# Kernel optimization log

Measured on AMD Instinct MI355X. Metric: run time of the kernel, lower is better.

## Reference

```python
import jax, jax.numpy as jnp
import numpy as np

B, T, C, H, K = 16, 8192, 128, 128, 5


def setup_inputs() -> dict:
    key = jax.random.key(0)
    ks = jax.random.split(key, 6)
    std = 1.0 / np.sqrt(H)  # matches reset_parameters uniform(-std, std)
    u = lambda k, s: jax.random.uniform(k, s, jnp.float32, -std, std)
    return {
        "inputs": jax.random.normal(ks[0], (B, T, C), jnp.float32),
        "init_state": jax.random.normal(ks[1], (2, B, H), jnp.float32),
        "z_w": u(ks[2], (H, C, K)),
        "z_b": u(ks[3], (H,)),
        "f_w": u(ks[4], (H, C, K)),
        "f_b": u(ks[5], (H,)),
    }


def _conv1d_same(x, w, b):
    # x: (B, C, T), w: (H, C, K) -> (B, H, T), padding='same'
    y = jax.lax.conv_general_dilated(
        x, w, window_strides=(1,), padding="SAME",
        dimension_numbers=("NCH", "OIH", "NCH"))
    return y + b[None, :, None]


def reference(inputs, init_state, z_w, z_b, f_w, f_b):
    # inputs: (B, T, C); init_state: (2, B, H)
    x = jnp.transpose(inputs, (0, 2, 1))                       # (B, C, T)
    raw_f = jnp.transpose(_conv1d_same(x, f_w, f_b), (0, 2, 1))  # (B, T, H)
    raw_z = jnp.transpose(_conv1d_same(x, z_w, z_b), (0, 2, 1))  # (B, T, H)
    # prepend init state along time -> (B, T+1, H)
    raw_f = jnp.concatenate([init_state[0][:, None, :], raw_f], axis=1)
    raw_z = jnp.concatenate([init_state[1][:, None, :], raw_z], axis=1)
    log_one_minus_f = jax.nn.log_sigmoid(-raw_f)  # mode='f'
    log_z = jax.nn.log_sigmoid(raw_z)
    log_f = jax.nn.log_sigmoid(raw_f)
    cs = jnp.cumsum(log_f, axis=1)
    # recurrent_gates[t] = log_f[t] - cumsum[t] + cumsum[-1]
    rg = log_f - cs + cs[:, -1:, :]
    log_hidden = jax.lax.cumlogsumexp(log_z + log_one_minus_f + rg, axis=1)
    return jnp.exp(log_hidden - rg)  # (B, T+1, H)
```

## Files before the change

### kernel.cpp

```cpp
#include <hip/hip_runtime.h>
#include <hip/hip_bf16.h>
#include <cstdint>

#define DEVFN __device__ __forceinline__

namespace {

constexpr int B = 16, T = 8192, C = 128, H = 128, K = 5;
constexpr int TP1 = T + 1;
constexpr int N = B * TP1 * H;
constexpr int NKK = 20;
constexpr int NCH = T / 64;
constexpr int NSER = B * H;
constexpr int WF_ELE = NKK * 8 * 64 * 2 * 8;
constexpr int XPITCH = 136;

typedef __attribute__((ext_vector_type(8))) short short8;
typedef __attribute__((ext_vector_type(4))) float f32x4;

DEVFN float sigmoidf(float x) { return 1.0f / (1.0f + __expf(-x)); }
DEVFN unsigned bfb(float v) {
  __hip_bfloat16 h = __float2bfloat16(v);
  return (unsigned)*reinterpret_cast<unsigned short*>(&h);
}

DEVFN void compose(float& P, float& Q, float& Fl, float Pr, float Qr, float Flr) {
  float t = Fl * Pr;
  P = P * t;
  Q = fmaf(t, Q, Qr);
  Fl = Flr;
}

__global__ __launch_bounds__(256)
void wprep_kernel(const float* __restrict__ fw, const float* __restrict__ zw,
                  short* __restrict__ Wfrag) {
  int idx = blockIdx.x * 256 + threadIdx.x;
  if (idx >= WF_ELE) return;
  int j = idx & 7;
  int fz = (idx >> 3) & 1;
  int lane = (idx >> 4) & 63;
  int nf8 = (idx >> 10) & 7;
  int kk = idx >> 13;
  int kdim = kk * 32 + ((lane >> 4) << 3) + j;
  int h = nf8 * 16 + (lane & 15);
  int k = kdim >> 7, c = kdim & 127;
  int src = (h * C + c) * K + k;
  float w = fz ? zw[src] : fw[src];
  Wfrag[idx] = (short)bfb(w);
}

__global__ __launch_bounds__(512, 4)
void conv_mfma_kernel(const float* __restrict__ x,
                      const float* __restrict__ fb, const float* __restrict__ zb,
                      const short* __restrict__ Wfrag,
                      unsigned* __restrict__ FG,
                      float* __restrict__ sumP, float* __restrict__ sumQ) {
  __shared__ short xs[68 * XPITCH];
  const int b = blockIdx.y;
  const int t0 = blockIdx.x * 64;
  const int tid = threadIdx.x;
  const int lane = tid & 63;
  const int wid = tid >> 6;
  const int lrow = lane & 15;
  const int lg = lane >> 4;

  for (int i = tid; i < 68 * 16; i += 512) {
    int r = i >> 4, co = (i & 15) << 3;
    int t = t0 - 2 + r;
    f32x4 v0 = {0.f, 0.f, 0.f, 0.f}, v1 = v0;
    if (t >= 0 && t < T) {
      const f32x4* p = reinterpret_cast<const f32x4*>(x + ((size_t)(b * T + t)) * C + co);
      v0 = p[0]; v1 = p[1];
    }
    short8 s;
    s[0] = (short)bfb(v0[0]); s[1] = (short)bfb(v0[1]); s[2] = (short)bfb(v0[2]); s[3] = (short)bfb(v0[3]);
    s[4] = (short)bfb(v1[0]); s[5] = (short)bfb(v1[1]); s[6] = (short)bfb(v1[2]); s[7] = (short)bfb(v1[3]);
    *reinterpret_cast<short8*>(xs + r * XPITCH + co) = s;
  }
  __syncthreads();

  f32x4 accF[4], accZ[4];
#pragma unroll
  for (int mf = 0; mf < 4; ++mf) { accF[mf] = {0.f,0.f,0.f,0.f}; accZ[mf] = {0.f,0.f,0.f,0.f}; }

  const char* xsb = reinterpret_cast<const char*>(xs);
  const short8* wb = reinterpret_cast<const short8*>(Wfrag) + (wid * 128 + lane * 2);
  const int abase = lrow * 272 + lg * 16;

  short8 wf[4], wz[4], av[2][4];
#pragma unroll
  for (int p = 0; p < 3; ++p) {
    wf[p] = wb[p * 1024];
    wz[p] = wb[p * 1024 + 1];
  }
#pragma unroll
  for (int mf = 0; mf < 4; ++mf)
    av[0][mf] = *reinterpret_cast<const short8*>(xsb + (abase + (mf * 16) * 272));

#pragma unroll
  for (int kk = 0; kk < NKK; ++kk) {
    __builtin_amdgcn_sched_barrier(0);
    if (kk + 3 < NKK) {
      const int o = (kk + 3) * 1024;
      wf[(kk + 3) & 3] = wb[o];
      wz[(kk + 3) & 3] = wb[o + 1];
    }
    if (kk + 1 < NKK) {
      const int k1 = (kk + 1) >> 2;
      const int cq1 = ((kk + 1) & 3) << 6;
#pragma unroll
      for (int mf = 0; mf < 4; ++mf)
        av[(kk + 1) & 1][mf] =
            *reinterpret_cast<const short8*>(xsb + (abase + (mf * 16 + k1) * 272 + cq1));
    }
    __builtin_amdgcn_sched_barrier(0);
#pragma unroll
    for (int mf = 0; mf < 4; ++mf) {
      accF[mf] = __builtin_amdgcn_mfma_f32_16x16x32_bf16(av[kk & 1][mf], wf[kk & 3], accF[mf], 0, 0, 0);
      accZ[mf] = __builtin_amdgcn_mfma_f32_16x16x32_bf16(av[kk & 1][mf], wz[kk & 3], accZ[mf], 0, 0, 0);
    }
  }

  const int cblk = blockIdx.x;
  const int h = wid * 16 + lrow;
  const float biasF = fb[h], biasZ = zb[h];
  float cP = 1.f, cQ = 0.f, cFl = 1.f;
#pragma unroll
  for (int mf = 0; mf < 4; ++mf) {
    float y = 0.f, P = 1.f, prevF = 1.f;
#pragma unroll
    for (int j = 0; j < 4; ++j) {
      int m = mf * 16 + lg * 4 + j;
      int s = t0 + m + 1;
      float rf = accF[mf][j] + biasF;
      float rz = accZ[mf][j] + biasZ;
      float F = sigmoidf(rf);
      float G = sigmoidf(rz) * (1.0f - F);
      FG[(size_t)(b * TP1 + s) * H + h] = bfb(F) | (bfb(G) << 16);
      if (j == 0) { y = G; P = 1.f; }
      else { P *= prevF; y = fmaf(prevF, y, G); }
      prevF = F;
    }
    float tP = P, tQ = y, tFl = prevF;
    {
      float pP = __shfl(tP, lane + 16, 64);
      float pQ = __shfl(tQ, lane + 16, 64);
      float pF = __shfl(tFl, lane + 16, 64);
      compose(tP, tQ, tFl, pP, pQ, pF);
      pP = __shfl(tP, lane + 32, 64);
      pQ = __shfl(tQ, lane + 32, 64);
      pF = __shfl(tFl, lane + 32, 64);
      compose(tP, tQ, tFl, pP, pQ, pF);
    }
    if (mf == 0) { cP = tP; cQ = tQ; cFl = tFl; }
    else compose(cP, cQ, cFl, tP, tQ, tFl);
  }
  if (lg == 0) {
    int sidx = cblk * NSER + b * H + h;
    sumP[sidx] = cP;
    sumQ[sidx] = cQ;
  }
}

__global__ void scanB_kernel(const float* __restrict__ init,
                             const unsigned* __restrict__ FG_r,
                             unsigned* __restrict__ FG_w,
                             const float* __restrict__ sumQ,
                             float* __restrict__ sumP_cin,
                             float* __restrict__ out) {
  int g = blockIdx.x * blockDim.x + threadIdx.x;
  int b = g >> 7, h = g & (H - 1);
  float rf = init[g];
  float rz = init[NSER + g];
  float F0 = sigmoidf(rf), z = sigmoidf(rz);
  float G0 = z * (1.0f - F0);
  size_t base = (size_t)b * TP1 * H + h;
  FG_w[base] = bfb(F0) | (bfb(G0) << 16);
  out[base] = G0;
  float y = G0;
  float prevFl = F0;
  for (int j = 0; j < NCH; ++j) {
    int sidx = j * NSER + g;
    float Ps = sumP_cin[sidx];
    float Q  = sumQ[sidx];
    sumP_cin[sidx] = y;
    y = fmaf(prevFl * Ps, y, Q);
    if (j + 1 < NCH)
      prevFl = __uint_as_float(FG_r[base + (size_t)(64 * (j + 1)) * H] << 16);
  }
}

__global__ __launch_bounds__(128)
void scanC_kernel(const unsigned* __restrict__ FG, const float* __restrict__ cin,
                  float* __restrict__ out) {
  const int b = blockIdx.y, j = blockIdx.x, h = threadIdx.x;
  const int s0 = 1 + j * 64;
  float y = cin[j * NSER + b * H + h];
  const size_t base = (size_t)b * TP1 * H + h;
  const unsigned* p = FG + base + (size_t)s0 * H;
  float Fprev = __uint_as_float(p[-H] << 16);
  float* po = out + base + (size_t)s0 * H;
#pragma unroll 8
  for (int t = 0; t < 64; ++t) {
    unsigned u = *p; p += H;
    float G = __uint_as_float(u & 0xffff0000u);
    y = fmaf(Fprev, y, G);
    Fprev = __uint_as_float(u << 16);
    *po = y; po += H;
  }
}

}

extern "C" void kernel_launch(void* const* d_in, const int* in_sizes, int n_in,
                              void* d_out, int out_size, void* d_ws, size_t ws_size,
                              hipStream_t stream) {
  const float* x    = (const float*)d_in[0];
  const float* init = (const float*)d_in[1];
  const float* zw   = (const float*)d_in[2];
  const float* zb   = (const float*)d_in[3];
  const float* fw   = (const float*)d_in[4];
  const float* fb   = (const float*)d_in[5];
  float* out = (float*)d_out;
  char* ws = (char*)d_ws;

  unsigned* FG = (unsigned*)ws;
  float* sumP = (float*)(ws + (size_t)N * 4);
  float* sumQ = sumP + (size_t)NCH * NSER;
  short* Wfrag = (short*)(sumQ + (size_t)NCH * NSER);

  wprep_kernel<<<(WF_ELE + 255) / 256, 256, 0, stream>>>(fw, zw, Wfrag);
  conv_mfma_kernel<<<dim3(NCH, B), 512, 0, stream>>>(x, fb, zb, Wfrag, FG, sumP, sumQ);
  scanB_kernel<<<16, 128, 0, stream>>>(init, FG, FG, sumQ, sumP, out);
  scanC_kernel<<<dim3(NCH, B), 128, 0, stream>>>(FG, sumP, out);
}
```

Measured before the change: 100.3 us.

## Fuse conv, chunk scan and apply into one cooperative kernel with grid syncs

Replaces the three-kernel conv/scanB/scanC sequence with a single cooperative kernel of 512 blocks. Each block computes four 64-step chunks, prefetching the next chunk's input into a double-buffered LDS tile. Grid syncs separate the conv phase, a serial carry scan over chunks done by four blocks, and the per-chunk apply phase. This removes kernel launch gaps and the extra FG reread in scanB. The cost is two grid-wide barriers, a serial scan running on only four blocks while the rest of the grid waits, and a dependence on cooperative-launch occupancy, with the old three-kernel path kept as a fallback.

Result: no change. 100.1 us (-0.2%).

```diff
diff --git a/kernel.cpp b/kernel.cpp
--- a/kernel.cpp
+++ b/kernel.cpp
@@ -1,5 +1,6 @@
 #include <hip/hip_runtime.h>
 #include <hip/hip_bf16.h>
+#include <hip/hip_cooperative_groups.h>
 #include <cstdint>
 
 #define DEVFN __device__ __forceinline__
@@ -14,6 +15,7 @@
 constexpr int NSER = B * H;
 constexpr int WF_ELE = NKK * 8 * 64 * 2 * 8;
 constexpr int XPITCH = 136;
+constexpr int XHALF = 68 * XPITCH;
 
 typedef __attribute__((ext_vector_type(8))) short short8;
 typedef __attribute__((ext_vector_type(4))) float f32x4;
@@ -47,6 +49,195 @@
   int src = (h * C + c) * K + k;
   float w = fz ? zw[src] : fw[src];
   Wfrag[idx] = (short)bfb(w);
+}
+
+DEVFN void stage_issue(const float* __restrict__ xp, int b, int t0, int tid,
+                       f32x4& a0, f32x4& b0, f32x4& a1, f32x4& b1,
+                       f32x4& a2, f32x4& b2) {
+  auto ld = [&](int i, f32x4& va, f32x4& vb) {
+    int r = i >> 4, co = (i & 15) << 3;
+    int t = t0 - 2 + r;
+    va = {0.f, 0.f, 0.f, 0.f}; vb = va;
+    if (t >= 0 && t < T) {
+      const f32x4* p = reinterpret_cast<const f32x4*>(xp + ((size_t)(b * T + t)) * C + co);
+      va = p[0]; vb = p[1];
+    }
+  };
+  ld(tid, a0, b0);
+  ld(tid + 512, a1, b1);
+  if (tid < 64) ld(tid + 1024, a2, b2);
+}
+DEVFN void stage_write(short* xsbuf, int tid,
+                       f32x4& a0, f32x4& b0, f32x4& a1, f32x4& b1,
+                       f32x4& a2, f32x4& b2) {
+  auto st = [&](int i, f32x4& va, f32x4& vb) {
+    int r = i >> 4, co = (i & 15) << 3;
+    short8 s;
+    s[0] = (short)bfb(va[0]); s[1] = (short)bfb(va[1]); s[2] = (short)bfb(va[2]); s[3] = (short)bfb(va[3]);
+    s[4] = (short)bfb(vb[0]); s[5] = (short)bfb(vb[1]); s[6] = (short)bfb(vb[2]); s[7] = (short)bfb(vb[3]);
+    *reinterpret_cast<short8*>(xsbuf + r * XPITCH + co) = s;
+  };
+  st(tid, a0, b0);
+  st(tid + 512, a1, b1);
+  if (tid < 64) st(tid + 1024, a2, b2);
+}
+
+__global__ __launch_bounds__(512, 4)
+void fused_kernel(const float* __restrict__ x,
+                  const float* __restrict__ fb, const float* __restrict__ zb,
+                  const float* __restrict__ initst,
+                  const short* __restrict__ Wfrag,
+                  float2* __restrict__ stat,
+                  unsigned* __restrict__ FG,
+                  float* __restrict__ out) {
+  __shared__ short xs[2 * XHALF];
+  const int bid = blockIdx.x;
+  const int b = bid >> 5;
+  const int q = bid & 31;
+  const int tid = threadIdx.x;
+  const int lane = tid & 63;
+  const int wid = tid >> 6;
+  const int lrow = lane & 15;
+  const int lg = lane >> 4;
+
+  const short8* wb = reinterpret_cast<const short8*>(Wfrag) + (wid * 128 + lane * 2);
+  const int abase = lrow * 272 + lg * 16;
+  const int h = wid * 16 + lrow;
+  const float biasF = fb[h], biasZ = zb[h];
+
+  f32x4 p0a, p0b, p1a, p1b, p2a, p2b;
+
+  stage_issue(x, b, q * 256, tid, p0a, p0b, p1a, p1b, p2a, p2b);
+  stage_write(xs, tid, p0a, p0b, p1a, p1b, p2a, p2b);
+  __syncthreads();
+
+#pragma unroll 1
+  for (int c = 0; c < 4; ++c) {
+    const int t0 = (q * 4 + c) * 64;
+    const char* xsb = reinterpret_cast<const char*>(xs + (c & 1) * XHALF);
+
+    f32x4 accF[4], accZ[4];
+#pragma unroll
+    for (int mf = 0; mf < 4; ++mf) { accF[mf] = {0.f,0.f,0.f,0.f}; accZ[mf] = {0.f,0.f,0.f,0.f}; }
+
+    short8 wf[4], wz[4], av[2][4];
+#pragma unroll
+    for (int p = 0; p < 3; ++p) {
+      wf[p] = wb[p * 1024];
+      wz[p] = wb[p * 1024 + 1];
+    }
+#pragma unroll
+    for (int mf = 0; mf < 4; ++mf)
+      av[0][mf] = *reinterpret_cast<const short8*>(xsb + (abase + (mf * 16) * 272));
+
+#pragma unroll
+    for (int kk = 0; kk < NKK; ++kk) {
+      __builtin_amdgcn_sched_barrier(0);
+      if (kk + 3 < NKK) {
+        const int o = (kk + 3) * 1024;
+        wf[(kk + 3) & 3] = wb[o];
+        wz[(kk + 3) & 3] = wb[o + 1];
+      }
+      if (kk + 1 < NKK) {
+        const int k1 = (kk + 1) >> 2;
+        const int cq1 = ((kk + 1) & 3) << 6;
+#pragma unroll
+        for (int mf = 0; mf < 4; ++mf)
+          av[(kk + 1) & 1][mf] =
+              *reinterpret_cast<const short8*>(xsb + (abase + (mf * 16 + k1) * 272 + cq1));
+      }
+      __builtin_amdgcn_sched_barrier(0);
+#pragma unroll
+      for (int mf = 0; mf < 4; ++mf) {
+        accF[mf] = __builtin_amdgcn_mfma_f32_16x16x32_bf16(av[kk & 1][mf], wf[kk & 3], accF[mf], 0, 0, 0);
+        accZ[mf] = __builtin_amdgcn_mfma_f32_16x16x32_bf16(av[kk & 1][mf], wz[kk & 3], accZ[mf], 0, 0, 0);
+      }
+    }
+
+    if (c < 3)
+      stage_issue(x, b, t0 + 64, tid, p0a, p0b, p1a, p1b, p2a, p2b);
+    __builtin_amdgcn_sched_barrier(0);
+
+    float cP = 1.f, cQ = 0.f, cFl = 1.f;
+#pragma unroll
+    for (int mf = 0; mf < 4; ++mf) {
+      float y = 0.f, P = 1.f, prevF = 1.f;
+#pragma unroll
+      for (int j = 0; j < 4; ++j) {
+        int m = mf * 16 + lg * 4 + j;
+        int s = t0 + m + 1;
+        float F = sigmoidf(accF[mf][j] + biasF);
+        float G = sigmoidf(accZ[mf][j] + biasZ) * (1.0f - F);
+        FG[(size_t)(b * TP1 + s) * H + h] = bfb(F) | (bfb(G) << 16);
+        if (j == 0) { y = G; P = 1.f; }
+        else { P *= prevF; y = fmaf(prevF, y, G); }
+        prevF = F;
+      }
+      float tP = P, tQ = y, tFl = prevF;
+      {
+        float pP = __shfl(tP, lane + 16, 64);
+        float pQ = __shfl(tQ, lane + 16, 64);
+        float pF = __shfl(tFl, lane + 16, 64);
+        compose(tP, tQ, tFl, pP, pQ, pF);
+        pP = __shfl(tP, lane + 32, 64);
+        pQ = __shfl(tQ, lane + 32, 64);
+        pF = __shfl(tFl, lane + 32, 64);
+        compose(tP, tQ, tFl, pP, pQ, pF);
+      }
+      if (mf == 0) { cP = tP; cQ = tQ; cFl = tFl; }
+      else compose(cP, cQ, cFl, tP, tQ, tFl);
+    }
+    if (lg == 0)
+      stat[(size_t)(b * NCH + q * 4 + c) * H + h] = make_float2(cP, cQ);
+
+    if (c < 3) {
+      __syncthreads();
+      stage_write(xs + ((c + 1) & 1) * XHALF, tid, p0a, p0b, p1a, p1b, p2a, p2b);
+      __syncthreads();
+    }
+  }
+
+  cooperative_groups::this_grid().sync();
+
+  if (bid < 4) {
+    int g = bid * 512 + tid;
+    int b2 = g >> 7, h2 = g & (H - 1);
+    float F0 = sigmoidf(initst[g]);
+    float z0 = sigmoidf(initst[NSER + g]);
+    float G0 = z0 * (1.0f - F0);
+    size_t base = (size_t)b2 * TP1 * H + h2;
+    out[base] = G0;
+    float y = G0, Fp = F0;
+    for (int j = 0; j < NCH; ++j) {
+      size_t sidx = (size_t)(b2 * NCH + j) * H + h2;
+      float2 pq = stat[sidx];
+      stat[sidx] = make_float2(y, Fp);
+      y = fmaf(Fp * pq.x, y, pq.y);
+      if (j + 1 < NCH)
+        Fp = __uint_as_float(FG[base + (size_t)(64 * (j + 1)) * H] << 16);
+    }
+  }
+
+  cooperative_groups::this_grid().sync();
+
+  {
+    const int sub = tid >> 7;
+    const int h3 = tid & (H - 1);
+    const int j = q * 4 + sub;
+    float2 cf = stat[(size_t)(b * NCH + j) * H + h3];
+    float y = cf.x, Fprev = cf.y;
+    size_t base = (size_t)b * TP1 * H + h3;
+    const unsigned* p = FG + base + (size_t)(1 + j * 64) * H;
+    float* po = out + base + (size_t)(1 + j * 64) * H;
+#pragma unroll 8
+    for (int t = 0; t < 64; ++t) {
+      unsigned u = *p; p += H;
+      float G = __uint_as_float(u & 0xffff0000u);
+      y = fmaf(Fprev, y, G);
+      Fprev = __uint_as_float(u << 16);
+      *po = y; po += H;
+    }
+  }
 }
 
 __global__ __launch_bounds__(512, 4)
@@ -224,13 +415,26 @@
   float* out = (float*)d_out;
   char* ws = (char*)d_ws;
 
-  unsigned* FG = (unsigned*)ws;
-  float* sumP = (float*)(ws + (size_t)N * 4);
-  float* sumQ = sumP + (size_t)NCH * NSER;
-  short* Wfrag = (short*)(sumQ + (size_t)NCH * NSER);
+  unsigned* FG  = (unsigned*)ws;
+  float2*  stat = (float2*)(ws + (size_t)N * 4);
+  float*   sumP = (float*)stat;
+  float*   sumQ = sumP + (size_t)NCH * NSER;
+  short*  Wfrag = (short*)(ws + (size_t)N * 4 + (size_t)NCH * NSER * 8);
 
   wprep_kernel<<<(WF_ELE + 255) / 256, 256, 0, stream>>>(fw, zw, Wfrag);
-  conv_mfma_kernel<<<dim3(NCH, B), 512, 0, stream>>>(x, fb, zb, Wfrag, FG, sumP, sumQ);
-  scanB_kernel<<<16, 128, 0, stream>>>(init, FG, FG, sumQ, sumP, out);
-  scanC_kernel<<<dim3(NCH, B), 128, 0, stream>>>(FG, sumP, out);
-}
+
+  bool coop = false;
+  int nb = 0;
+  if (hipOccupancyMaxActiveBlocksPerMultiprocessor(
+          &nb, (const void*)fused_kernel, 512, 0) == hipSuccess && nb >= 2) {
+    void* args[] = {(void*)&x, (void*)&fb, (void*)&zb, (void*)&init,
+                    (void*)&Wfrag, (void*)&stat, (void*)&FG, (void*)&out};
+    coop = hipLaunchCooperativeKernel((const void*)fused_kernel, dim3(512), dim3(512),
+                                      args, 0, stream) == hipSuccess;
+  }
+  if (!coop) {
+    conv_mfma_kernel<<<dim3(NCH, B), 512, 0, stream>>>(x, fb, zb, Wfrag, FG, sumP, sumQ);
+    scanB_kernel<<<16, 128, 0, stream>>>(init, FG, FG, sumQ, sumP, out);
+    scanC_kernel<<<dim3(NCH, B), 128, 0, stream>>>(FG, sumP, out);
+  }
+}
```
